# Optimization experiments

Hardware: AMD Instinct MI355X
Metric: run time of the kernel (lower is better)

Reference implementation:

```python
import jax, jax.numpy as jnp
import numpy as np

IMG_SIZE = 224
PATCH_SIZE = 16
CONTEXT_LEN = 316
LATENT_DIM = 1024
NUM_HEADS = 16
NUM_PATCHES = (IMG_SIZE // PATCH_SIZE) ** 2  # 196
SEQ_LEN = NUM_PATCHES + CONTEXT_LEN          # 512
BATCH = 8


def prefix_lm_mask(num_img_patches, total):
    # lower-triangular causal mask, but the image-patch block is fully bidirectional
    m = np.tril(np.ones((total, total), dtype=np.float32))
    m[:num_img_patches, :num_img_patches] = 1.0
    return jnp.asarray(m)  # [S, S], 1 = attend, 0 = masked


def setup_inputs() -> dict:
    key = jax.random.key(0)
    k_x, k_q, k_k, k_v, k_o, k_b = jax.random.split(key, 6)
    d = LATENT_DIM
    scale = 1.0 / np.sqrt(d)
    return {
        "x": jax.random.normal(k_x, (BATCH, SEQ_LEN, d), dtype=jnp.float32),
        "w_q": jax.random.normal(k_q, (d, d), dtype=jnp.float32) * scale,
        "w_k": jax.random.normal(k_k, (d, d), dtype=jnp.float32) * scale,
        "w_v": jax.random.normal(k_v, (d, d), dtype=jnp.float32) * scale,
        "w_o": jax.random.normal(k_o, (d, d), dtype=jnp.float32) * scale,
        "b_o": jax.random.normal(k_b, (d,), dtype=jnp.float32) * 0.01,
    }


def reference(x, w_q, w_k, w_v, w_o, b_o):
    B, S, D = x.shape
    H = NUM_HEADS
    hd = D // H
    # projections (nn.Linear: y = x @ W^T)
    q = (x @ w_q.T).reshape(B, S, H, hd).transpose(0, 2, 1, 3)  # [B,H,S,hd]
    k = (x @ w_k.T).reshape(B, S, H, hd).transpose(0, 2, 1, 3)
    v = (x @ w_v.T).reshape(B, S, H, hd).transpose(0, 2, 1, 3)
    scores = jnp.einsum("bhqd,bhkd->bhqk", q, k) / jnp.sqrt(jnp.float32(hd))
    mask = prefix_lm_mask(NUM_PATCHES, S)  # [S,S]
    scores = jnp.where(mask == 0, jnp.float32(-jnp.inf), scores)
    attn = jax.nn.softmax(scores, axis=-1)
    ctx = jnp.einsum("bhqk,bhkd->bhqd", attn, v)
    ctx = ctx.transpose(0, 2, 1, 3).reshape(B, S, D)
    return ctx @ w_o.T + b_o
```

## Files before the change

### kernel.cpp

```cpp
#include <hip/hip_runtime.h>
#include <stdint.h>
#include <math.h>

#define NB_B 8
#define NB_S 512
#define NB_D 1024
#define NB_H 16
#define NB_HD 64
#define NP 196
#define MTOT 4096

#define OFF_XB 0
#define OFF_WQ 4194304
#define OFF_WK 5242880
#define OFF_WV 6291456
#define OFF_WO 7340032
#define OFF_Q  8388608
#define OFF_K  12582912
#define OFF_VT 16777216
#define OFF_CT 20971520

typedef __attribute__((ext_vector_type(8))) short bf16x8;
typedef __attribute__((ext_vector_type(4))) float f32x4;
typedef __attribute__((ext_vector_type(4))) short s16x4;
typedef __attribute__((ext_vector_type(8))) short s16x8;

__device__ __forceinline__ short f2bf(float f) {
  union { float f; uint32_t u; } c; c.f = f;
  uint32_t r = (c.u + 0x7fffu + ((c.u >> 16) & 1u)) >> 16;
  return (short)r;
}

__device__ __forceinline__ uint32_t pack2bf(float lo, float hi) {
  uint32_t ulo = __float_as_uint(lo) + 0x8000u;
  uint32_t uhi = __float_as_uint(hi) + 0x8000u;
  return __builtin_amdgcn_perm(uhi, ulo, 0x07060302u);
}

__device__ __forceinline__ void async16(void* lds, const void* g) {
  __builtin_amdgcn_global_load_lds(
      (const __attribute__((address_space(1))) void*)g,
      (__attribute__((address_space(3))) void*)lds, 16, 0, 0);
}

__global__ __launch_bounds__(256) void cvt5(const float* __restrict__ x,
                                            const float* __restrict__ wq,
                                            const float* __restrict__ wk,
                                            const float* __restrict__ wv,
                                            const float* __restrict__ wo,
                                            short* __restrict__ ws) {
  int b = blockIdx.x, t = threadIdx.x;
  const float* src; short* dst; float scale;
  if (b < 256) {
    src = x + b * 16384;
    dst = ws + OFF_XB + b * 16384;
    scale = 1.0f;
  } else {
    int wi = (b - 256) >> 6, gn = (b - 256) & 63;
    const float* wsrc[4] = {wq, wk, wv, wo};
    src = wsrc[wi] + gn * 16384;
    dst = ws + OFF_WQ + wi * 1048576 + gn * 16384;
    scale = (wi == 0) ? 0.125f : 1.0f;
  }
#pragma unroll
  for (int it = 0; it < 8; ++it) {
    int s = t + it * 256;
    int kb = s >> 6, l = s & 63, quad = l >> 4, cc = l & 15;
    const float* sp = src + cc * 1024 + kb * 32 + quad * 8;
    float4 v0 = *(const float4*)sp;
    float4 v1 = *(const float4*)(sp + 4);
    s16x8 o;
    o[0] = f2bf(v0.x * scale); o[1] = f2bf(v0.y * scale);
    o[2] = f2bf(v0.z * scale); o[3] = f2bf(v0.w * scale);
    o[4] = f2bf(v1.x * scale); o[5] = f2bf(v1.y * scale);
    o[6] = f2bf(v1.z * scale); o[7] = f2bf(v1.w * scale);
    *(s16x8*)(dst + s * 8) = o;
  }
}

__global__ __launch_bounds__(256, 2) void gemm_qkv(short* __restrict__ ws) {
  __shared__ __align__(16) short As[4096];
  __shared__ __align__(16) short Bs[4096];
  int bx = blockIdx.x;
  int wsel = bx >> 8;
  int tile = bx & 255;
  int mt = tile >> 3, nt = tile & 7;
  int m0 = mt << 7, n0 = nt << 7;
  const short* A  = ws + OFF_XB;
  const short* Bw = ws + OFF_WQ + wsel * 1048576;
  int t = threadIdx.x, lane = t & 63, wvi = t >> 6;
  int c = lane & 15, quad = lane >> 4;
  int wm = wvi >> 1, wn = wvi & 1;
  int g0 = mt << 3, gn0 = nt << 3;
  f32x4 acc[4][4] = {};

  for (int kk = 0; kk < 1024; kk += 32) {
    int kb = kk >> 5;
#pragma unroll
    for (int i = 0; i < 2; ++i) {
      int ch = wvi * 2 + i;
      async16(&As[ch << 9], A  + ((g0  + ch) * 32 + kb) * 512 + lane * 8);
      async16(&Bs[ch << 9], Bw + ((gn0 + ch) * 32 + kb) * 512 + lane * 8);
    }
    __syncthreads();
    bf16x8 af[4], bfr[4];
#pragma unroll
    for (int i = 0; i < 4; ++i) af[i]  = *(const bf16x8*)&As[((wm * 4 + i) << 9) + lane * 8];
#pragma unroll
    for (int j = 0; j < 4; ++j) bfr[j] = *(const bf16x8*)&Bs[((wn * 4 + j) << 9) + lane * 8];
#pragma unroll
    for (int i = 0; i < 4; ++i)
#pragma unroll
      for (int j = 0; j < 4; ++j)
        acc[i][j] = __builtin_amdgcn_mfma_f32_16x16x32_bf16(af[i], bfr[j], acc[i][j], 0, 0, 0);
    __syncthreads();
  }

#pragma unroll
  for (int i = 0; i < 4; ++i) {
#pragma unroll
    for (int j = 0; j < 4; ++j) {
      int n = n0 + wn * 64 + j * 16 + c;
      int h = n >> 6, d = n & 63;
      int mq = m0 + wm * 64 + i * 16 + quad * 4;
      int bb = mq >> 9, srow = mq & 511;
      if (wsel == 0) {
        short* outp = ws + OFF_Q;
#pragma unroll
        for (int r = 0; r < 4; ++r)
          outp[((bb * 16 + h) * 512 + srow + r) * 64 + d] = f2bf(acc[i][j][r]);
      } else if (wsel == 1) {
        int dblk = d >> 5, qk = (d >> 3) & 3, jd = d & 7;
        int kg = srow >> 4;
        size_t base = (size_t)(bb * 16 + h) * 32768 +
                      (size_t)(((kg * 2 + dblk) * 64 + qk * 16 + quad * 4)) * 8 + jd;
        short* outp = ws + OFF_K;
#pragma unroll
        for (int r = 0; r < 4; ++r) outp[base + r * 8] = f2bf(acc[i][j][r]);
      } else {
        int dg = d >> 4, cv = d & 15;
        int kblk = srow >> 5, qv = (srow >> 3) & 3, jv = srow & 7;
        s16x4 o;
#pragma unroll
        for (int r = 0; r < 4; ++r) o[r] = f2bf(acc[i][j][r]);
        *(s16x4*)&ws[OFF_VT + (size_t)(bb * 16 + h) * 32768 +
                     (size_t)((dg * 16 + kblk) * 64 + qv * 16 + cv) * 8 + jv] = o;
      }
    }
  }
}

__global__ __launch_bounds__(256, 2) void attn(short* __restrict__ ws) {
  __shared__ __align__(16) short Kb[4096];
  __shared__ __align__(16) short Vb[4096];
  int bi = blockIdx.x;
  int bh = bi >> 2, qcr = bi & 3;
  int qc = (qcr + bh + 2 * (bh >> 6)) & 3;
  int t = threadIdx.x, lane = t & 63, wvi = t >> 6;
  int c = lane & 15, quad = lane >> 4;
  const short* Qh   = ws + OFF_Q  + bh * (512 * 64);
  const short* Ksw  = ws + OFF_K  + (size_t)bh * 32768;
  const short* Vsw  = ws + OFF_VT + (size_t)bh * 32768;
  short* ct = ws + OFF_CT;
  int b = bh >> 4, h = bh & 15;

  int qt0 = qc * 128 + wvi * 32;
  int qt1 = qt0 + 16;
  int kn0 = (qt0 + 16 > NP) ? (qt0 + 16) : NP;
  int kn1 = (qt1 + 16 > NP) ? (qt1 + 16) : NP;
  int knb = (qc * 128 + 128 > NP) ? (qc * 128 + 128) : NP;
  int NCH = (knb + 63) >> 6;

  bf16x8 q00 = *(const bf16x8*)(Qh + (qt0 + c) * 64 + (quad << 3));
  bf16x8 q01 = *(const bf16x8*)(Qh + (qt0 + c) * 64 + 32 + (quad << 3));
  bf16x8 q10 = *(const bf16x8*)(Qh + (qt1 + c) * 64 + (quad << 3));
  bf16x8 q11 = *(const bf16x8*)(Qh + (qt1 + c) * 64 + 32 + (quad << 3));

  f32x4 acc0[4] = {}, acc1[4] = {};
  float l0 = 0.0f, l1 = 0.0f;
  int L0 = c + ((quad & 1) << 5);
  bool hilo = quad >= 2;

  for (int ch = 0; ch < NCH; ++ch) {
    int k0 = ch << 6;
    {
      int kg = (k0 >> 4) + wvi;
#pragma unroll
      for (int f = 0; f < 2; ++f)
        async16(&Kb[(wvi * 2 + f) << 9], Ksw + ((kg * 2 + f) * 512) + lane * 8);
      int kblk = k0 >> 5;
#pragma unroll
      for (int f = 0; f < 2; ++f)
        async16(&Vb[(wvi * 2 + f) << 9], Vsw + ((wvi * 16 + kblk + f) * 512) + lane * 8);
    }
    __syncthreads();

    bf16x8 ak[4][2], av[4][2];
#pragma unroll
    for (int mb = 0; mb < 4; ++mb)
#pragma unroll
      for (int f = 0; f < 2; ++f) {
        ak[mb][f] = *(const bf16x8*)&Kb[((mb * 2 + f) << 9) + lane * 8];
        av[mb][f] = *(const bf16x8*)&Vb[((mb * 2 + f) << 9) + lane * 8];
      }

#pragma unroll
    for (int s = 0; s < 2; ++s) {
      int qt = s ? qt1 : qt0;
      int kn = s ? kn1 : kn0;
      if (k0 >= kn) continue;
      bf16x8 bq0 = s ? q10 : q00;
      bf16x8 bq1 = s ? q11 : q01;
      f32x4* acc = s ? acc1 : acc0;

      float p[4][4];
#pragma unroll
      for (int mb = 0; mb < 4; ++mb) {
        f32x4 st = {};
        st = __builtin_amdgcn_mfma_f32_16x16x32_bf16(ak[mb][0], bq0, st, 0, 0, 0);
        st = __builtin_amdgcn_mfma_f32_16x16x32_bf16(ak[mb][1], bq1, st, 0, 0, 0);
#pragma unroll
        for (int r = 0; r < 4; ++r) p[mb][r] = __expf(st[r]);
      }

      if ((k0 + 64 > NP) && (k0 + 64 > qt + 1)) {
        int row = qt + c;
#pragma unroll
        for (int mb = 0; mb < 4; ++mb)
#pragma unroll
          for (int r = 0; r < 4; ++r) {
            int key = k0 + mb * 16 + (quad << 2) + r;
            bool v = (row < NP) ? (key < NP) : (key <= row);
            p[mb][r] = v ? p[mb][r] : 0.0f;
          }
      }
      float ls = 0.0f;
#pragma unroll
      for (int mb = 0; mb < 4; ++mb)
#pragma unroll
        for (int r = 0; r < 4; ++r) ls += p[mb][r];
      if (s) l1 += ls; else l0 += ls;

#pragma unroll
      for (int hh = 0; hh < 2; ++hh) {
        float* pa = p[2 * hh];
        float* pb = p[2 * hh + 1];
        uint32_t e0 = pack2bf(pa[0], pa[1]);
        uint32_t e1 = pack2bf(pa[2], pa[3]);
        uint32_t e2 = pack2bf(pb[0], pb[1]);
        uint32_t e3 = pack2bf(pb[2], pb[3]);
        uint32_t a0 = (uint32_t)__shfl((int)e0, L0);
        uint32_t b0 = (uint32_t)__shfl((int)e1, L0);
        uint32_t a1 = (uint32_t)__shfl((int)e0, L0 + 16);
        uint32_t b1 = (uint32_t)__shfl((int)e1, L0 + 16);
        uint32_t c0 = (uint32_t)__shfl((int)e2, L0);
        uint32_t d0 = (uint32_t)__shfl((int)e3, L0);
        uint32_t c1 = (uint32_t)__shfl((int)e2, L0 + 16);
        uint32_t d1 = (uint32_t)__shfl((int)e3, L0 + 16);
        union { uint32_t u[4]; bf16x8 v; } bp;
        bp.u[0] = hilo ? c0 : a0;
        bp.u[1] = hilo ? d0 : b0;
        bp.u[2] = hilo ? c1 : a1;
        bp.u[3] = hilo ? d1 : b1;
#pragma unroll
        for (int db = 0; db < 4; ++db)
          acc[db] = __builtin_amdgcn_mfma_f32_16x16x32_bf16(av[db][hh], bp.v, acc[db], 0, 0, 0);
      }
    }
    __syncthreads();
  }

#pragma unroll
  for (int s = 0; s < 2; ++s) {
    float l = s ? l1 : l0;
    f32x4* acc = s ? acc1 : acc0;
    int qt = s ? qt1 : qt0;
    l += __shfl_xor(l, 16);
    l += __shfl_xor(l, 32);
    float inv = 1.0f / l;
    int g = (b * 512 + qt) >> 4;
#pragma unroll
    for (int db = 0; db < 4; ++db) {
      int col0 = h * 64 + db * 16 + quad * 4;
      int kb = col0 >> 5, qp = (col0 & 31) >> 3, jo = col0 & 7;
      s16x4 o;
#pragma unroll
      for (int r = 0; r < 4; ++r) o[r] = f2bf(acc[db][r] * inv);
      *(s16x4*)&ct[(size_t)((g * 32 + kb) * 64 + qp * 16 + c) * 8 + jo] = o;
    }
  }
}

__global__ __launch_bounds__(256, 2) void gemm_out(const short* __restrict__ ws,
                                                   const float* __restrict__ bias,
                                                   float* __restrict__ out) {
  __shared__ __align__(16) short As[4096];
  __shared__ __align__(16) short Bs[8192];
  int bx = blockIdx.x;
  int mt = bx >> 3, nt = bx & 7;
  int m0 = mt << 6, n0 = nt << 7;
  const short* A  = ws + OFF_CT;
  const short* Bw = ws + OFF_WO;
  int t = threadIdx.x, lane = t & 63, wvi = t >> 6;
  int c = lane & 15, quad = lane >> 4;
  int wm = wvi >> 1, wn = wvi & 1;
  int g0 = m0 >> 4, gn0 = n0 >> 4;
  f32x4 acc[2][4] = {};

  for (int kk = 0; kk < 1024; kk += 64) {
    int kb = kk >> 5;
#pragma unroll
    for (int i = 0; i < 6; ++i) {
      int ch = wvi * 6 + i;
      if (ch < 8) {
        int mg = ch >> 1, kh = ch & 1;
        async16(&As[ch << 9], A + ((g0 + mg) * 32 + kb + kh) * 512 + lane * 8);
      } else {
        int cb = ch - 8, mg = cb >> 1, kh = cb & 1;
        async16(&Bs[cb << 9], Bw + ((gn0 + mg) * 32 + kb + kh) * 512 + lane * 8);
      }
    }
    __syncthreads();

    bf16x8 af[2][2], bfr[4][2];
#pragma unroll
    for (int i = 0; i < 2; ++i)
#pragma unroll
      for (int kh = 0; kh < 2; ++kh)
        af[i][kh] = *(const bf16x8*)&As[((((wm * 2 + i) << 1) + kh) << 9) + lane * 8];
#pragma unroll
    for (int j = 0; j < 4; ++j)
#pragma unroll
      for (int kh = 0; kh < 2; ++kh)
        bfr[j][kh] = *(const bf16x8*)&Bs[((((wn * 4 + j) << 1) + kh) << 9) + lane * 8];
#pragma unroll
    for (int kh = 0; kh < 2; ++kh)
#pragma unroll
      for (int i = 0; i < 2; ++i)
#pragma unroll
        for (int j = 0; j < 4; ++j)
          acc[i][j] = __builtin_amdgcn_mfma_f32_16x16x32_bf16(af[i][kh], bfr[j][kh], acc[i][j], 0, 0, 0);
    __syncthreads();
  }

#pragma unroll
  for (int j = 0; j < 4; ++j) {
    int n = n0 + wn * 64 + j * 16 + c;
    float bj = bias[n];
#pragma unroll
    for (int i = 0; i < 2; ++i) {
      int mq = m0 + wm * 32 + i * 16 + quad * 4;
#pragma unroll
      for (int r = 0; r < 4; ++r)
        out[(size_t)(mq + r) * 1024 + n] = acc[i][j][r] + bj;
    }
  }
}

extern "C" void kernel_launch(void* const* d_in, const int* in_sizes, int n_in,
                              void* d_out, int out_size, void* d_ws, size_t ws_size,
                              hipStream_t stream) {
  (void)in_sizes; (void)n_in; (void)out_size; (void)ws_size;
  const float* x  = (const float*)d_in[0];
  const float* wq = (const float*)d_in[1];
  const float* wk = (const float*)d_in[2];
  const float* wv = (const float*)d_in[3];
  const float* wo = (const float*)d_in[4];
  const float* bo = (const float*)d_in[5];
  short* ws = (short*)d_ws;
  float* out = (float*)d_out;

  cvt5<<<512, 256, 0, stream>>>(x, wq, wk, wv, wo, ws);
  gemm_qkv<<<768, 256, 0, stream>>>(ws);
  attn<<<512, 256, 0, stream>>>(ws);
  gemm_out<<<512, 256, 0, stream>>>(ws, bo, out);
}
```

Before: 156.5 us.

## Stage fp32-to-bf16 conversion through LDS and store Q in swizzled MFMA layout

The conversion kernel now reads each fp32 tile with fully coalesced float4 loads, packs to bf16 into a padded LDS buffer, and then emits the MFMA-swizzled layout from LDS. Previously each thread gathered strided 32-byte segments straight from global memory. Q is now written by the QKV GEMM in the same fragment-swizzled layout as K, so attention loads Q fragments with contiguous per-lane reads. This adds about 32KB of LDS per conversion block, which may lower occupancy, and the Q epilogue becomes scattered 2-byte stores.

```diff
diff --git a/kernel.cpp b/kernel.cpp
--- a/kernel.cpp
+++ b/kernel.cpp
@@ -49,6 +49,7 @@
                                             const float* __restrict__ wv,
                                             const float* __restrict__ wo,
                                             short* __restrict__ ws) {
+  __shared__ uint32_t lt[16 * 513];
   int b = blockIdx.x, t = threadIdx.x;
   const float* src; short* dst; float scale;
   if (b < 256) {
@@ -57,24 +58,36 @@
     scale = 1.0f;
   } else {
     int wi = (b - 256) >> 6, gn = (b - 256) & 63;
-    const float* wsrc[4] = {wq, wk, wv, wo};
-    src = wsrc[wi] + gn * 16384;
+    switch (wi) {
+      case 0:  src = wq + gn * 16384; scale = 0.125f; break;
+      case 1:  src = wk + gn * 16384; scale = 1.0f;   break;
+      case 2:  src = wv + gn * 16384; scale = 1.0f;   break;
+      default: src = wo + gn * 16384; scale = 1.0f;   break;
+    }
     dst = ws + OFF_WQ + wi * 1048576 + gn * 16384;
-    scale = (wi == 0) ? 0.125f : 1.0f;
-  }
-#pragma unroll
-  for (int it = 0; it < 8; ++it) {
-    int s = t + it * 256;
+  }
+#pragma unroll
+  for (int i = 0; i < 16; ++i) {
+    int flat = t + i * 256;
+    int row = flat >> 8, col4 = flat & 255;
+    float4 v = *(const float4*)(src + flat * 4);
+    uint32_t lo = (uint32_t)(uint16_t)f2bf(v.x * scale) |
+                  ((uint32_t)(uint16_t)f2bf(v.y * scale) << 16);
+    uint32_t hi = (uint32_t)(uint16_t)f2bf(v.z * scale) |
+                  ((uint32_t)(uint16_t)f2bf(v.w * scale) << 16);
+    lt[row * 513 + col4 * 2]     = lo;
+    lt[row * 513 + col4 * 2 + 1] = hi;
+  }
+  __syncthreads();
+#pragma unroll
+  for (int i = 0; i < 8; ++i) {
+    int s = t + i * 256;
     int kb = s >> 6, l = s & 63, quad = l >> 4, cc = l & 15;
-    const float* sp = src + cc * 1024 + kb * 32 + quad * 8;
-    float4 v0 = *(const float4*)sp;
-    float4 v1 = *(const float4*)(sp + 4);
-    s16x8 o;
-    o[0] = f2bf(v0.x * scale); o[1] = f2bf(v0.y * scale);
-    o[2] = f2bf(v0.z * scale); o[3] = f2bf(v0.w * scale);
-    o[4] = f2bf(v1.x * scale); o[5] = f2bf(v1.y * scale);
-    o[6] = f2bf(v1.z * scale); o[7] = f2bf(v1.w * scale);
-    *(s16x8*)(dst + s * 8) = o;
+    int base = cc * 513 + kb * 16 + quad * 4;
+    union { uint32_t u[4]; s16x8 v; } o;
+    o.u[0] = lt[base];     o.u[1] = lt[base + 1];
+    o.u[2] = lt[base + 2]; o.u[3] = lt[base + 3];
+    *(s16x8*)(dst + s * 8) = o.v;
   }
 }
 
@@ -124,17 +137,12 @@
       int h = n >> 6, d = n & 63;
       int mq = m0 + wm * 64 + i * 16 + quad * 4;
       int bb = mq >> 9, srow = mq & 511;
-      if (wsel == 0) {
-        short* outp = ws + OFF_Q;
-#pragma unroll
-        for (int r = 0; r < 4; ++r)
-          outp[((bb * 16 + h) * 512 + srow + r) * 64 + d] = f2bf(acc[i][j][r]);
-      } else if (wsel == 1) {
+      if (wsel < 2) {
         int dblk = d >> 5, qk = (d >> 3) & 3, jd = d & 7;
-        int kg = srow >> 4;
+        int g = srow >> 4;
+        short* outp = ws + (wsel == 0 ? OFF_Q : OFF_K);
         size_t base = (size_t)(bb * 16 + h) * 32768 +
-                      (size_t)(((kg * 2 + dblk) * 64 + qk * 16 + quad * 4)) * 8 + jd;
-        short* outp = ws + OFF_K;
+                      (size_t)(((g * 2 + dblk) * 64 + qk * 16 + quad * 4)) * 8 + jd;
 #pragma unroll
         for (int r = 0; r < 4; ++r) outp[base + r * 8] = f2bf(acc[i][j][r]);
       } else {
@@ -158,7 +166,7 @@
   int qc = (qcr + bh + 2 * (bh >> 6)) & 3;
   int t = threadIdx.x, lane = t & 63, wvi = t >> 6;
   int c = lane & 15, quad = lane >> 4;
-  const short* Qh   = ws + OFF_Q  + bh * (512 * 64);
+  const short* Qsw  = ws + OFF_Q  + (size_t)bh * 32768;
   const short* Ksw  = ws + OFF_K  + (size_t)bh * 32768;
   const short* Vsw  = ws + OFF_VT + (size_t)bh * 32768;
   short* ct = ws + OFF_CT;
@@ -171,10 +179,11 @@
   int knb = (qc * 128 + 128 > NP) ? (qc * 128 + 128) : NP;
   int NCH = (knb + 63) >> 6;
 
-  bf16x8 q00 = *(const bf16x8*)(Qh + (qt0 + c) * 64 + (quad << 3));
-  bf16x8 q01 = *(const bf16x8*)(Qh + (qt0 + c) * 64 + 32 + (quad << 3));
-  bf16x8 q10 = *(const bf16x8*)(Qh + (qt1 + c) * 64 + (quad << 3));
-  bf16x8 q11 = *(const bf16x8*)(Qh + (qt1 + c) * 64 + 32 + (quad << 3));
+  int qg0 = qt0 >> 4, qg1 = qt1 >> 4;
+  bf16x8 q00 = *(const bf16x8*)(Qsw + ((qg0 * 2 + 0) * 64 + lane) * 8);
+  bf16x8 q01 = *(const bf16x8*)(Qsw + ((qg0 * 2 + 1) * 64 + lane) * 8);
+  bf16x8 q10 = *(const bf16x8*)(Qsw + ((qg1 * 2 + 0) * 64 + lane) * 8);
+  bf16x8 q11 = *(const bf16x8*)(Qsw + ((qg1 * 2 + 1) * 64 + lane) * 8);
 
   f32x4 acc0[4] = {}, acc1[4] = {};
   float l0 = 0.0f, l1 = 0.0f;
```

Result: no change. 153.7 us (-1.8%).
